# Performance work log

Hardware: AMD Instinct MI355X
Metric: run time of the kernel (lower is better)

The kernel has to match this reference:

```python
import jax, jax.numpy as jnp
import numpy as np

# NVFP4 E2M1 representable magnitudes and decision midpoints (round-to-nearest)
_E2M1_GRID = np.array([0.0, 0.5, 1.0, 1.5, 2.0, 3.0, 4.0, 6.0], dtype=np.float32)
_E2M1_MIDS = np.array([0.25, 0.75, 1.25, 1.75, 2.5, 3.5, 5.0], dtype=np.float32)
_BLOCK = 16  # quant_tile_shape=(1,16)


def fake_quant_nvfp4(t):
    """Blockwise (16 contiguous elems) E2M1 fake quant with pow2 scales."""
    shape = t.shape
    v = t.reshape(-1, _BLOCK)                      # [n_blocks, 16]
    amax = jnp.max(jnp.abs(v), axis=-1, keepdims=True)
    # power-of-2 scale so that amax/scale <= 6 (E2M1 max)
    exp = jnp.ceil(jnp.log2(jnp.maximum(amax, jnp.float32(1e-30)) / 6.0))
    scale = jnp.where(amax > 0, jnp.exp2(exp), jnp.float32(1.0))
    u = v / scale
    a = jnp.abs(u)
    grid = jnp.asarray(_E2M1_GRID, dtype=t.dtype)
    mids = jnp.asarray(_E2M1_MIDS, dtype=t.dtype)
    idx = jnp.digitize(a, mids)                    # nearest E2M1 magnitude index
    q = jnp.sign(u) * grid[idx]
    return (q * scale).reshape(shape)


def setup_inputs() -> dict:
    key = jax.random.key(0)
    kx, kw = jax.random.split(key)
    x = jax.random.normal(kx, (32, 256, 64, 64), dtype=jnp.float32)
    w = jax.random.normal(kw, (256, 256, 3, 3), dtype=jnp.float32) * 0.05
    return {"x": x, "w": w}


def reference(x, w):
    qx = fake_quant_nvfp4(x)
    qw = fake_quant_nvfp4(w)
    # conv2d, stride 1, padding 1, no bias, NCHW / OIHW
    return jax.lax.conv_general_dilated(
        qx, qw,
        window_strides=(1, 1),
        padding=((1, 1), (1, 1)),
        dimension_numbers=("NCHW", "OIHW", "NCHW"),
    )
```

## Files before the change

kernel.cpp:

```cpp
#include <hip/hip_runtime.h>
#include <stdint.h>

typedef __attribute__((ext_vector_type(8))) short short8;
typedef __attribute__((ext_vector_type(4))) float f32x4;

#define N_IMG 32
#define C_IN  256
#define HH    64
#define WW    64
#define O_OUT 256
#define HP    66
#define WP    66

#define QX_ELEMS (N_IMG*HP*WP*C_IN)
#define QX_BYTES ((size_t)QX_ELEMS*2)
#define QW_ELEMS (9*O_OUT*C_IN)


__device__ __forceinline__ float e2m1_mag(float a) {
    return a < 0.25f ? 0.0f
         : a < 0.75f ? 0.5f
         : a < 1.25f ? 1.0f
         : a < 1.75f ? 1.5f
         : a < 2.5f  ? 2.0f
         : a < 3.5f  ? 3.0f
         : a < 5.0f  ? 4.0f : 6.0f;
}

__device__ __forceinline__ void blk_scale2(float amax, float& s, float& inv) {
    float ac = fmaxf(amax, 1e-30f);
    int e;
    float m = frexpf(ac, &e);
    int ex = (m > 0.75f) ? (e - 2) : (e - 3);
    if (amax > 0.0f) { s = ldexpf(1.0f, ex); inv = ldexpf(1.0f, -ex); }
    else             { s = 1.0f; inv = 1.0f; }
}

__device__ __forceinline__ unsigned short to_bf16_bits(float v) {
    union { float f; unsigned int u; } cv; cv.f = v;
    return (unsigned short)(cv.u >> 16);
}

__global__ __launch_bounds__(256) void halo_zero_kernel(unsigned short* __restrict__ qx) {
    int id = blockIdx.x * 256 + threadIdx.x;
    size_t off;
    if (id < 135168) {
        int n = id / 4224, r = id % 4224;
        int h = (r / 2112) * 65;
        int k = r % 2112;
        off = (((size_t)(n*HP + h)) * WP) * C_IN + (size_t)k * 8;
    } else {
        int j = id - 135168;
        int n = j >> 12, r = j & 4095;
        int h = 1 + (r >> 6);
        int w = ((r >> 5) & 1) * 65;
        int k = r & 31;
        off = (((size_t)(n*HP + h)) * WP + w) * C_IN + (size_t)k * 8;
    }
    uint4 z; z.x = z.y = z.z = z.w = 0u;
    *(uint4*)(qx + off) = z;
}

__global__ __launch_bounds__(256) void quant_x_kernel(const float* __restrict__ x,
                                                      unsigned short* __restrict__ qx) {
    __shared__ float xf[64][65];
    __shared__ float sarr[4][65];
    __shared__ float iarr[4][65];

    const int bid = blockIdx.x;
    const int n  = bid >> 8;
    const int h  = (bid >> 2) & 63;
    const int cb = bid & 3;
    const int t  = threadIdx.x;

    {
        const int rb = t >> 4;
        const int w4 = (t & 15) * 4;
        const float* src = x + (((size_t)(n*C_IN + cb*64)) * HH + h) * WW;
#pragma unroll
        for (int it = 0; it < 4; ++it) {
            int r = it * 16 + rb;
            float4 g = *(const float4*)(src + (size_t)r * (HH*WW) + w4);
            xf[r][w4+0] = g.x; xf[r][w4+1] = g.y; xf[r][w4+2] = g.z; xf[r][w4+3] = g.w;
        }
    }
    __syncthreads();

    {
        const int c = t >> 2, wb = t & 3;
        float amax = 0.f;
#pragma unroll
        for (int j = 0; j < 16; ++j) amax = fmaxf(amax, fabsf(xf[c][wb*16 + j]));
        float s, inv;
        blk_scale2(amax, s, inv);
        sarr[wb][c] = s;
        iarr[wb][c] = inv;
    }
    __syncthreads();

    {
        const int w = t >> 2, cg = (t & 3) * 16, wb = w >> 4;
        unsigned short outv[16];
#pragma unroll
        for (int i = 0; i < 16; ++i) {
            int c = cg + i;
            float v = xf[c][w];
            float q = copysignf(e2m1_mag(fabsf(v) * iarr[wb][c]) * sarr[wb][c], v);
            outv[i] = to_bf16_bits(q);
        }
        unsigned short* dst = qx + (((size_t)(n*HP + h + 1)) * WP + (w + 1)) * C_IN + cb*64 + cg;
        *(uint4*)(dst)     = *(const uint4*)&outv[0];
        *(uint4*)(dst + 8) = *(const uint4*)&outv[8];
    }
}

__global__ __launch_bounds__(256) void quant_w_kernel(const float* __restrict__ w,
                                                      unsigned short* __restrict__ qw) {
    __shared__ unsigned short lq[2304];
    const int o = blockIdx.x;
    const int t = threadIdx.x;
    const float* src = w + (size_t)o * 2304;
    if (t < 144) {
        float v[16];
#pragma unroll
        for (int j = 0; j < 4; ++j) {
            float4 f = ((const float4*)(src + t*16))[j];
            v[j*4+0]=f.x; v[j*4+1]=f.y; v[j*4+2]=f.z; v[j*4+3]=f.w;
        }
        float amax = 0.f;
#pragma unroll
        for (int j = 0; j < 16; ++j) amax = fmaxf(amax, fabsf(v[j]));
        float s, inv;
        blk_scale2(amax, s, inv);
#pragma unroll
        for (int j = 0; j < 16; ++j)
            lq[t*16 + j] = to_bf16_bits(copysignf(e2m1_mag(fabsf(v[j]) * inv) * s, v[j]));
    }
    __syncthreads();
#pragma unroll
    for (int p = 0; p < 9; ++p)
        qw[((size_t)(p*O_OUT + o)) * C_IN + t] = lq[t*9 + p];
}

__device__ __forceinline__ void gld16(void* lds, const void* g) {
    __builtin_amdgcn_global_load_lds(
        (const __attribute__((address_space(1))) unsigned int*)g,
        (__attribute__((address_space(3))) unsigned int*)lds,
        16, 0, 0);
}

__global__ __launch_bounds__(256) void conv_kernel(const unsigned short* __restrict__ qw,
                                                   const unsigned short* __restrict__ qx,
                                                   float* __restrict__ out) {
    __shared__ unsigned short Wt[128][32];
    __shared__ unsigned short Xt[128][32];

    const int tid  = threadIdx.x;
    const int wave = tid >> 6;
    const int lane = tid & 63;
    const int lo16 = lane & 15;
    const int quad = lane >> 4;

    const int id  = blockIdx.x;
    const int g   = id >> 3;
    const int n   = ((g >> 6) << 3) | (id & 7);
    const int j_  = g & 63;
    const int o0  = (j_ & 1) * 128;
    const int hw0 = (j_ >> 1) * 128;
    const int h0  = hw0 >> 6;

    const int s0 = wave * 2;
    const int r0 = s0 * 16 + (lane >> 2);
    const int r1 = r0 + 16;
    const int co = (lane & 3) * 8;

    const unsigned short* wb0 = qw + (size_t)(o0 + r0) * C_IN + co;
    const unsigned short* wb1 = qw + (size_t)(o0 + r1) * C_IN + co;

    auto xbase = [&](int r) -> const unsigned short* {
        int h = h0 + (r >> 6);
        int w = r & 63;
        return qx + (((size_t)(n*HP + h + 1)) * WP + (w + 1)) * C_IN + co;
    };
    const unsigned short* xb0 = xbase(r0);
    const unsigned short* xb1 = xbase(r1);

    unsigned short* ldsA0 = &Wt[s0*16][0];
    unsigned short* ldsA1 = &Wt[s0*16 + 16][0];
    unsigned short* ldsB0 = &Xt[s0*16][0];
    unsigned short* ldsB1 = &Xt[s0*16 + 16][0];

    const int wmo = (wave & 1) * 64;
    const int wnp = (wave >> 1) * 64;

    f32x4 acc[4][4];
#pragma unroll
    for (int i = 0; i < 4; ++i)
#pragma unroll
        for (int j = 0; j < 4; ++j)
            acc[i][j] = (f32x4){0.f, 0.f, 0.f, 0.f};

    for (int p = 0; p < 9; ++p) {
        const int dh = p/3 - 1, dw = p%3 - 1;
        const int xoff = (dh*WP + dw) * C_IN;
        const int woff = p * (O_OUT * C_IN);
        for (int cc = 0; cc < 8; ++cc) {
            const int c0 = cc * 32;
            gld16(ldsA0, wb0 + woff + c0);
            gld16(ldsA1, wb1 + woff + c0);
            gld16(ldsB0, xb0 + xoff + c0);
            gld16(ldsB1, xb1 + xoff + c0);
            __syncthreads();

            short8 af[4], bf_[4];
#pragma unroll
            for (int i = 0; i < 4; ++i)
                af[i] = *(const short8*)&Wt[wmo + i*16 + lo16][quad*8];
#pragma unroll
            for (int j = 0; j < 4; ++j)
                bf_[j] = *(const short8*)&Xt[wnp + j*16 + lo16][quad*8];
#pragma unroll
            for (int i = 0; i < 4; ++i)
#pragma unroll
                for (int j = 0; j < 4; ++j)
                    acc[i][j] = __builtin_amdgcn_mfma_f32_16x16x32_bf16(
                        af[i], bf_[j], acc[i][j], 0, 0, 0);
            __syncthreads();
        }
    }

#pragma unroll
    for (int i = 0; i < 4; ++i) {
#pragma unroll
        for (int j = 0; j < 4; ++j) {
            int o  = o0 + wmo + i*16 + quad*4;
            int pl = wnp + j*16 + lo16;
            size_t base = ((size_t)(n*O_OUT + o)) * (HH*WW) + hw0 + pl;
#pragma unroll
            for (int r = 0; r < 4; ++r)
                out[base + (size_t)r*(HH*WW)] = acc[i][j][r];
        }
    }
}

extern "C" void kernel_launch(void* const* d_in, const int* in_sizes, int n_in,
                              void* d_out, int out_size, void* d_ws, size_t ws_size,
                              hipStream_t stream) {
    const float* x = (const float*)d_in[0];
    const float* w = (const float*)d_in[1];
    float* out = (float*)d_out;

    unsigned short* qx = (unsigned short*)d_ws;
    unsigned short* qw = (unsigned short*)((char*)d_ws + QX_BYTES);

    halo_zero_kernel<<<dim3(1040), 256, 0, stream>>>(qx);
    quant_x_kernel<<<dim3(N_IMG*HH*4), 256, 0, stream>>>(x, qx);
    quant_w_kernel<<<dim3(O_OUT), 256, 0, stream>>>(w, qw);
    conv_kernel<<<dim3(2048), 256, 0, stream>>>(qw, qx, out);
}
```

Baseline: 432.3 us.

## Rework conv kernel into 256x256 tiles with double-buffered swizzled LDS pipeline

The implicit-GEMM conv kernel now uses 512-thread blocks, each computing all 256 output channels for 256 pixels, with K chunks of 64 channels. It double-buffers 128KB of LDS and issues the next tile's global-to-LDS loads in phases interleaved with MFMA work, with manual vmcnt waits, barriers and setprio. LDS rows use XOR swizzling to avoid bank conflicts. The goal is to hide memory latency and raise data reuse per block, at the cost of fewer blocks (512), heavy register use (128 accumulators per lane) and fragile hand-tuned synchronisation.

```diff
diff --git a/kernel.cpp b/kernel.cpp
--- a/kernel.cpp
+++ b/kernel.cpp
@@ -1,5 +1,6 @@
 #include <hip/hip_runtime.h>
 #include <stdint.h>
+#include <stddef.h>
 
 typedef __attribute__((ext_vector_type(8))) short short8;
 typedef __attribute__((ext_vector_type(4))) float f32x4;
@@ -149,96 +150,143 @@
         16, 0, 0);
 }
 
-__global__ __launch_bounds__(256) void conv_kernel(const unsigned short* __restrict__ qw,
+__device__ __forceinline__ short8 rd8(const void* p) {
+    return *(const short8*)p;
+}
+
+#define MFMA16 __builtin_amdgcn_mfma_f32_16x16x32_bf16
+
+#define MM16(I0, A00, A01, A10, A11)                                      \
+    do {                                                                  \
+        _Pragma("unroll")                                                 \
+        for (int j = 0; j < 4; ++j) {                                     \
+            acc[I0][j]     = MFMA16(A00, b[j][0], acc[I0][j],     0,0,0); \
+            acc[I0][j]     = MFMA16(A01, b[j][1], acc[I0][j],     0,0,0); \
+            acc[(I0)+1][j] = MFMA16(A10, b[j][0], acc[(I0)+1][j], 0,0,0); \
+            acc[(I0)+1][j] = MFMA16(A11, b[j][1], acc[(I0)+1][j], 0,0,0); \
+        }                                                                 \
+    } while (0)
+
+#define PHASE(Q, S1, S2, VM)                                              \
+    do {                                                                  \
+        short8 aa0 = rd8(LA + rA + (2*(Q))*2048   + cA0);                 \
+        short8 aa1 = rd8(LA + rA + (2*(Q))*2048   + (cA0^64));            \
+        short8 aa2 = rd8(LA + rA + (2*(Q)+1)*2048 + cA0);                 \
+        short8 aa3 = rd8(LA + rA + (2*(Q)+1)*2048 + (cA0^64));            \
+        S1; S2;                                                           \
+        __builtin_amdgcn_s_barrier();                                     \
+        asm volatile("s_waitcnt lgkmcnt(0)" ::: "memory");                \
+        __builtin_amdgcn_sched_barrier(0);                                \
+        __builtin_amdgcn_s_setprio(1);                                    \
+        MM16(2*(Q), aa0, aa1, aa2, aa3);                                  \
+        __builtin_amdgcn_s_setprio(0);                                    \
+        asm volatile("s_waitcnt " VM ::: "memory");                       \
+        __builtin_amdgcn_s_barrier();                                     \
+    } while (0)
+
+__global__ __launch_bounds__(512) void conv_kernel(const unsigned short* __restrict__ qw,
                                                    const unsigned short* __restrict__ qx,
                                                    float* __restrict__ out) {
-    __shared__ unsigned short Wt[128][32];
-    __shared__ unsigned short Xt[128][32];
+    __shared__ unsigned short lds[65536];
+    char* Lc = (char*)lds;
 
     const int tid  = threadIdx.x;
-    const int wave = tid >> 6;
+    const int w    = tid >> 6;
     const int lane = tid & 63;
     const int lo16 = lane & 15;
     const int quad = lane >> 4;
+    const int wm   = w & 1;
+    const int wn   = w >> 1;
 
     const int id  = blockIdx.x;
-    const int g   = id >> 3;
-    const int n   = ((g >> 6) << 3) | (id & 7);
-    const int j_  = g & 63;
-    const int o0  = (j_ & 1) * 128;
-    const int hw0 = (j_ >> 1) * 128;
-    const int h0  = hw0 >> 6;
-
-    const int s0 = wave * 2;
-    const int r0 = s0 * 16 + (lane >> 2);
-    const int r1 = r0 + 16;
-    const int co = (lane & 3) * 8;
-
-    const unsigned short* wb0 = qw + (size_t)(o0 + r0) * C_IN + co;
-    const unsigned short* wb1 = qw + (size_t)(o0 + r1) * C_IN + co;
-
-    auto xbase = [&](int r) -> const unsigned short* {
-        int h = h0 + (r >> 6);
-        int w = r & 63;
-        return qx + (((size_t)(n*HP + h + 1)) * WP + (w + 1)) * C_IN + co;
-    };
-    const unsigned short* xb0 = xbase(r0);
-    const unsigned short* xb1 = xbase(r1);
-
-    unsigned short* ldsA0 = &Wt[s0*16][0];
-    unsigned short* ldsA1 = &Wt[s0*16 + 16][0];
-    unsigned short* ldsB0 = &Xt[s0*16][0];
-    unsigned short* ldsB1 = &Xt[s0*16 + 16][0];
-
-    const int wmo = (wave & 1) * 64;
-    const int wnp = (wave >> 1) * 64;
-
-    f32x4 acc[4][4];
-#pragma unroll
-    for (int i = 0; i < 4; ++i)
+    const int idx = id >> 3;
+    const int n   = (id & 7) + ((idx >> 4) << 3);
+    const int pt  = idx & 15;
+    const int h0  = pt * 4;
+    const int hw0 = pt * 256;
+
+    const int trow  = tid >> 3;
+    const int c_off = ((tid & 7) ^ (trow & 7)) << 3;
+    const unsigned short* gB = qx + ((size_t)((n*HP + h0 + 1) * WP + trow + 1)) * C_IN + c_off;
+    const int ro0 = trow + ((tid >= 256) ? 96 : 0);
+    const unsigned short* gA = qw + (size_t)ro0 * C_IN + c_off;
+    const int awb = w * 1024 + ((w < 4) ? 0 : 12288);
+    const int bwb = w * 1024;
+
+    const int key = (lo16 & 7) << 4;
+    const int cA0 = (quad << 4) ^ key;
+    const int rA  = (wm * 128 + lo16) * 128;
+    const int rB  = (wn * 64  + lo16) * 128;
+
+    f32x4 acc[8][4];
+#pragma unroll
+    for (int i = 0; i < 8; ++i)
 #pragma unroll
         for (int j = 0; j < 4; ++j)
             acc[i][j] = (f32x4){0.f, 0.f, 0.f, 0.f};
 
-    for (int p = 0; p < 9; ++p) {
-        const int dh = p/3 - 1, dw = p%3 - 1;
-        const int xoff = (dh*WP + dw) * C_IN;
-        const int woff = p * (O_OUT * C_IN);
-        for (int cc = 0; cc < 8; ++cc) {
-            const int c0 = cc * 32;
-            gld16(ldsA0, wb0 + woff + c0);
-            gld16(ldsA1, wb1 + woff + c0);
-            gld16(ldsB0, xb0 + xoff + c0);
-            gld16(ldsB1, xb1 + xoff + c0);
-            __syncthreads();
-
-            short8 af[4], bf_[4];
-#pragma unroll
-            for (int i = 0; i < 4; ++i)
-                af[i] = *(const short8*)&Wt[wmo + i*16 + lo16][quad*8];
-#pragma unroll
-            for (int j = 0; j < 4; ++j)
-                bf_[j] = *(const short8*)&Xt[wnp + j*16 + lo16][quad*8];
-#pragma unroll
-            for (int i = 0; i < 4; ++i)
-#pragma unroll
-                for (int j = 0; j < 4; ++j)
-                    acc[i][j] = __builtin_amdgcn_mfma_f32_16x16x32_bf16(
-                        af[i], bf_[j], acc[i][j], 0, 0, 0);
-            __syncthreads();
-        }
-    }
-
-#pragma unroll
-    for (int i = 0; i < 4; ++i) {
+    {
+        const unsigned short* ga = gA;
+        const unsigned short* gb = gB - 17152;
+        char* SA = Lc;
+        char* SB = Lc + 32768;
+        gld16(SB + bwb,         gb);
+        gld16(SB + bwb + 8192,  gb + 16896);
+        gld16(SB + bwb + 16384, gb + 2*16896);
+        gld16(SB + bwb + 24576, gb + 3*16896);
+        gld16(SA + awb,         ga);
+        gld16(SA + awb + 4096,  ga + 8192);
+        gld16(SA + awb + 8192,  ga + 16384);
+        gld16(SA + awb + 12288, ga + 24576);
+        asm volatile("s_waitcnt vmcnt(0)" ::: "memory");
+        __builtin_amdgcn_s_barrier();
+    }
+
+    int curOff = 0;
+#pragma unroll 1
+    for (int t = 0; t < 36; ++t) {
+        const int tn  = (t < 35) ? (t + 1) : 35;
+        const int pn  = tn >> 2;
+        const int qn  = pn / 3;
+        const int dwn = pn - qn * 3;
+        const int cn  = (tn & 3) << 6;
+        const unsigned short* ga = gA + pn * 65536 + cn;
+        const unsigned short* gb = gB + (ptrdiff_t)((qn - 1) * WP + (dwn - 1)) * C_IN + cn;
+
+        const char* LA = Lc + curOff;
+        const char* LB = LA + 32768;
+        char* SA = Lc + (curOff ^ 65536);
+        char* SB = SA + 32768;
+
+        short8 b[4][2];
 #pragma unroll
         for (int j = 0; j < 4; ++j) {
-            int o  = o0 + wmo + i*16 + quad*4;
-            int pl = wnp + j*16 + lo16;
-            size_t base = ((size_t)(n*O_OUT + o)) * (HH*WW) + hw0 + pl;
+            b[j][0] = rd8(LB + rB + j*2048 + cA0);
+            b[j][1] = rd8(LB + rB + j*2048 + (cA0^64));
+        }
+
+        PHASE(0, gld16(SB + bwb,         gb),
+                 gld16(SB + bwb + 8192,  gb + 16896),   "vmcnt(4)");
+        PHASE(1, gld16(SB + bwb + 16384, gb + 2*16896),
+                 gld16(SB + bwb + 24576, gb + 3*16896), "vmcnt(5)");
+        PHASE(2, gld16(SA + awb,         ga),
+                 gld16(SA + awb + 4096,  ga + 8192),    "vmcnt(6)");
+        PHASE(3, gld16(SA + awb + 8192,  ga + 16384),
+                 gld16(SA + awb + 12288, ga + 24576),   "vmcnt(3)");
+
+        curOff ^= 65536;
+    }
+
+#pragma unroll
+    for (int i = 0; i < 8; ++i) {
+        const int o = wm * 128 + i * 16 + quad * 4;
+        float* orow = out + ((size_t)(n * O_OUT + o)) * (HH*WW) + hw0 + wn * 64 + lo16;
+#pragma unroll
+        for (int j = 0; j < 4; ++j) {
+            float* dst = orow + j * 16;
 #pragma unroll
             for (int r = 0; r < 4; ++r)
-                out[base + (size_t)r*(HH*WW)] = acc[i][j][r];
+                dst[(size_t)r * (HH*WW)] = acc[i][j][r];
         }
     }
 }
@@ -256,5 +304,5 @@
     halo_zero_kernel<<<dim3(1040), 256, 0, stream>>>(qx);
     quant_x_kernel<<<dim3(N_IMG*HH*4), 256, 0, stream>>>(x, qx);
     quant_w_kernel<<<dim3(O_OUT), 256, 0, stream>>>(w, qw);
-    conv_kernel<<<dim3(2048), 256, 0, stream>>>(qw, qx, out);
-}
+    conv_kernel<<<dim3(512), 512, 0, stream>>>(qw, qx, out);
+}
```

Measured after the change: 363.3 us. 15.9% less time.
